# Kernel optimization log

Hardware: AMD Instinct MI355X
Metric: run time of the kernel (lower is better)

## Reference

```python
import jax, jax.numpy as jnp
import numpy as np

N_HEADS = 16
EMBED_DIM = 2048
BATCH, SEQ = 2, 2048


def setup_inputs() -> dict:
    key = jax.random.key(0)
    k1, k2, k3, k4, k5 = jax.random.split(key, 5)
    s_in = 1.0 / np.sqrt(EMBED_DIM)
    return {
        "x": jax.random.normal(k1, (BATCH, SEQ, EMBED_DIM), dtype=jnp.float32),
        "w_in": jax.random.normal(k2, (3 * EMBED_DIM, EMBED_DIM), dtype=jnp.float32) * s_in,
        "b_in": jax.random.normal(k3, (3 * EMBED_DIM,), dtype=jnp.float32) * 0.02,
        "w_out": jax.random.normal(k4, (EMBED_DIM, EMBED_DIM), dtype=jnp.float32) * s_in,
        "b_out": jax.random.normal(k5, (EMBED_DIM,), dtype=jnp.float32) * 0.02,
        "causal_mask": 1,
    }


def reference(x, w_in, b_in, w_out, b_out, causal_mask):
    b, l, e = x.shape
    h, d = N_HEADS, e // N_HEADS
    qkv = x @ w_in.T + b_in                      # [b, l, 3e]
    q, k, v = jnp.split(qkv, 3, axis=-1)
    # b l (h d) -> b h l d
    q = q.reshape(b, l, h, d).transpose(0, 2, 1, 3)
    k = k.reshape(b, l, h, d).transpose(0, 2, 1, 3)
    v = v.reshape(b, l, h, d).transpose(0, 2, 1, 3)
    scores = jnp.einsum("bhqd,bhkd->bhqk", q, k) / jnp.sqrt(jnp.float32(d))
    if causal_mask:
        tri = jnp.triu(jnp.ones((l, l), dtype=bool), k=1)  # True above diagonal
        scores = jnp.where(tri, -jnp.inf, scores)
    attn = jax.nn.softmax(scores, axis=-1)
    out = jnp.einsum("bhqk,bhkd->bhqd", attn, v)  # [b, h, l, d]
    out = out.transpose(0, 2, 1, 3).reshape(b, l, e)
    return out @ w_out.T + b_out
```

## Files before the change

kernel.cpp:

```cpp
#include <hip/hip_runtime.h>
#include <hip/hip_bf16.h>
#include <math.h>

typedef __attribute__((ext_vector_type(4))) float floatx4;
typedef __attribute__((ext_vector_type(16))) float floatx16;
typedef __attribute__((ext_vector_type(8))) __bf16 bf16x8;

__device__ __forceinline__ unsigned short f2bf(float f) {
    union { float f; unsigned int u; } v; v.f = f;
    unsigned int u = v.u;
    u += 0x7FFFu + ((u >> 16) & 1u);
    return (unsigned short)(u >> 16);
}

__device__ __forceinline__ unsigned int pkbf(float a, float b) {
    return (unsigned int)f2bf(a) | ((unsigned int)f2bf(b) << 16);
}

__device__ __forceinline__ void gl_lds16(const void* g, void* l) {
    __builtin_amdgcn_global_load_lds(
        (const __attribute__((address_space(1))) void*)g,
        (__attribute__((address_space(3))) void*)l, 16, 0, 0);
}

__global__ void cast_f32_bf16(const float* __restrict__ in,
                              unsigned short* __restrict__ out, int n) {
    int i = (blockIdx.x * blockDim.x + threadIdx.x) * 4;
    if (i + 4 <= n) {
        float4 f = *(const float4*)(in + i);
        ushort4 o;
        o.x = f2bf(f.x); o.y = f2bf(f.y); o.z = f2bf(f.z); o.w = f2bf(f.w);
        *(ushort4*)(out + i) = o;
    }
}

#define BM 128
#define BN 128
#define BK 32
#define GROUP_M 8

template<int MODE>
__global__ __launch_bounds__(256) void gemm_nt(
    const unsigned short* __restrict__ A,
    const unsigned short* __restrict__ B,
    const float* __restrict__ bias,
    float* __restrict__ Cf,
    unsigned short* __restrict__ q_ws,
    unsigned short* __restrict__ k_ws,
    unsigned short* __restrict__ vT_ws,
    int M, int N, int K)
{
    __shared__ unsigned short Asm[BM][BK];
    __shared__ unsigned short Bsm[BN][BK];

    const int id = blockIdx.x + gridDim.x * blockIdx.y;
    const int perGroup = gridDim.x * GROUP_M;
    const int group = id / perGroup;
    const int rem = id % perGroup;
    const int gh = min(GROUP_M, (int)gridDim.y - group * GROUP_M);
    const int by = group * GROUP_M + rem % gh;
    const int bx = rem / gh;

    const int m0 = by * BM, n0 = bx * BN;
    const int tid = threadIdx.x;
    const int lane = tid & 63, wid = tid >> 6;
    const int quad = lane >> 4, li = lane & 15;
    const int wy = wid >> 1, wx = wid & 1;

    const int lrow = lane >> 2;
    const int lcol = (lane & 3) * 8;

    floatx4 acc[4][4] = {};

    const int kTiles = K / BK;
    for (int kt = 0; kt < kTiles; ++kt) {
        const int k0 = kt * BK;
        #pragma unroll
        for (int c = 0; c < 2; ++c) {
            const int cidx = wid * 2 + c;
            const int row = cidx * 16 + lrow;
            gl_lds16(A + (size_t)(m0 + row) * K + k0 + lcol,
                     &Asm[0][0] + cidx * 512);
            gl_lds16(B + (size_t)(n0 + row) * K + k0 + lcol,
                     &Bsm[0][0] + cidx * 512);
        }
        __syncthreads();

        bf16x8 af[4], bfr[4];
        #pragma unroll
        for (int t = 0; t < 4; ++t) {
            af[t]  = *(const bf16x8*)(&Asm[wy * 64 + t * 16 + li][quad * 8]);
            bfr[t] = *(const bf16x8*)(&Bsm[wx * 64 + t * 16 + li][quad * 8]);
        }
        #pragma unroll
        for (int i = 0; i < 4; ++i)
            #pragma unroll
            for (int j = 0; j < 4; ++j)
                acc[i][j] = __builtin_amdgcn_mfma_f32_16x16x32_bf16(
                    af[i], bfr[j], acc[i][j], 0, 0, 0);
        __syncthreads();
    }

    if (MODE == 0) {
        #pragma unroll
        for (int i = 0; i < 4; ++i)
            #pragma unroll
            for (int j = 0; j < 4; ++j) {
                int col = wx * 64 + j * 16 + li;
                float bv = bias[n0 + col];
                #pragma unroll
                for (int r = 0; r < 4; ++r) {
                    int row = wy * 64 + i * 16 + quad * 4 + r;
                    Cf[(size_t)(m0 + row) * N + n0 + col] = acc[i][j][r] + bv;
                }
            }
    } else {
        const int which = bx >> 4;
        const int h = bx & 15;
        const int b = by >> 4;
        const int lbase = (by & 15) * BM;
        const size_t bh = (size_t)(b * 16 + h);
        #pragma unroll
        for (int i = 0; i < 4; ++i)
            #pragma unroll
            for (int j = 0; j < 4; ++j) {
                int col = wx * 64 + j * 16 + li;
                float bv = bias[n0 + col];
                #pragma unroll
                for (int r = 0; r < 4; ++r) {
                    int row = wy * 64 + i * 16 + quad * 4 + r;
                    int l = lbase + row;
                    unsigned short ob = f2bf(acc[i][j][r] + bv);
                    if (which == 0)      q_ws[(bh * 2048 + l) * 128 + col] = ob;
                    else if (which == 1) k_ws[(bh * 2048 + l) * 128 + col] = ob;
                    else                 vT_ws[(bh * 128 + col) * 2048 + l] = ob;
                }
            }
    }
}

#define AP 8
__global__ __launch_bounds__(256, 2) void attn_kernel(
    const unsigned short* __restrict__ q_ws,
    const unsigned short* __restrict__ k_ws,
    const unsigned short* __restrict__ vT_ws,
    unsigned short* __restrict__ aout,
    const int* __restrict__ causal_ptr)
{
    __shared__ unsigned short Ksm[128][128 + AP];
    __shared__ unsigned short Vsm[128][128 + AP];

    const int ord = blockIdx.x;
    int qt, bhid;
    if (ord < 256) { qt = ord >> 5;              bhid = ord & 31; }
    else           { qt = 15 - ((ord - 256) >> 5); bhid = ord & 31; }
    const int b = bhid >> 4, h = bhid & 15;

    const int tid = threadIdx.x;
    const int lane = tid & 63, w = tid >> 6;
    const int lq = lane & 31;
    const int half = lane >> 5;
    const size_t bh = (size_t)(b * 16 + h);
    const unsigned short* Qp = q_ws + bh * 2048 * 128;
    const unsigned short* Kp = k_ws + bh * 2048 * 128;
    const unsigned short* Vp = vT_ws + bh * 128 * 2048;
    const int causal = causal_ptr[0];
    const float scale = 0.08838834764831845f;

    const int qg = qt * 128 + w * 32 + lq;
    bf16x8 qf[8];
    #pragma unroll
    for (int s = 0; s < 8; ++s)
        qf[s] = *(const bf16x8*)(Qp + (size_t)qg * 128 + s * 16 + half * 8);

    floatx16 O[4] = {};
    float m_i = -INFINITY, l_i = 0.f;

    const int myEnd = causal ? qt : 15;
    for (int kt = 0; kt <= myEnd; ++kt) {
        #pragma unroll
        for (int c = 0; c < 8; ++c) {
            int chunk = c * 256 + tid;
            int row = chunk >> 4;
            int cc  = (chunk & 15) * 8;
            *(uint4*)(&Ksm[row][cc]) =
                *(const uint4*)(Kp + (size_t)(kt * 128 + row) * 128 + cc);
            *(uint4*)(&Vsm[row][cc]) =
                *(const uint4*)(Vp + (size_t)row * 2048 + kt * 128 + cc);
        }
        __syncthreads();

        floatx16 S[4] = {};
        #pragma unroll
        for (int ct = 0; ct < 4; ++ct)
            #pragma unroll
            for (int s = 0; s < 8; ++s) {
                bf16x8 kf = *(const bf16x8*)(&Ksm[ct * 32 + lq][s * 16 + half * 8]);
                S[ct] = __builtin_amdgcn_mfma_f32_32x32x16_bf16(kf, qf[s], S[ct], 0, 0, 0);
            }

        const bool diag = causal && (kt == qt);
        float mx = -INFINITY;
        #pragma unroll
        for (int ct = 0; ct < 4; ++ct)
            #pragma unroll
            for (int r = 0; r < 16; ++r) {
                float sv = S[ct][r] * scale;
                if (diag) {
                    int key = 32 * ct + (r & 3) + 8 * (r >> 2) + 4 * half;
                    if (kt * 128 + key > qg) sv = -INFINITY;
                }
                S[ct][r] = sv;
                mx = fmaxf(mx, sv);
            }
        mx = fmaxf(mx, __shfl_xor(mx, 32, 64));
        float m_new = fmaxf(m_i, mx);
        float m_use = (m_new == -INFINITY) ? 0.f : m_new;
        float alpha = __expf(m_i - m_use);

        float rs = 0.f;
        #pragma unroll
        for (int ct = 0; ct < 4; ++ct)
            #pragma unroll
            for (int r = 0; r < 16; ++r) {
                float p = __expf(S[ct][r] - m_use);
                S[ct][r] = p;
                rs += p;
            }
        rs += __shfl_xor(rs, 32, 64);
        l_i = l_i * alpha + rs;
        m_i = m_new;
        #pragma unroll
        for (int dt = 0; dt < 4; ++dt)
            #pragma unroll
            for (int r = 0; r < 16; ++r)
                O[dt][r] *= alpha;

        bf16x8 pfr[8];
        #pragma unroll
        for (int ct = 0; ct < 4; ++ct)
            #pragma unroll
            for (int h2 = 0; h2 < 2; ++h2) {
                int base = 8 * h2;
                unsigned int pk0 = pkbf(S[ct][base + 0], S[ct][base + 1]);
                unsigned int pk1 = pkbf(S[ct][base + 2], S[ct][base + 3]);
                unsigned int pk2 = pkbf(S[ct][base + 4], S[ct][base + 5]);
                unsigned int pk3 = pkbf(S[ct][base + 6], S[ct][base + 7]);
                unsigned int x0 = __shfl_xor((int)pk0, 32, 64);
                unsigned int x1 = __shfl_xor((int)pk1, 32, 64);
                unsigned int x2 = __shfl_xor((int)pk2, 32, 64);
                unsigned int x3 = __shfl_xor((int)pk3, 32, 64);
                union { unsigned int u[4]; bf16x8 v; } fr;
                fr.u[0] = half ? x2 : pk0;
                fr.u[1] = half ? x3 : pk1;
                fr.u[2] = half ? pk2 : x0;
                fr.u[3] = half ? pk3 : x1;
                pfr[ct * 2 + h2] = fr.v;
            }

        #pragma unroll
        for (int dt = 0; dt < 4; ++dt)
            #pragma unroll
            for (int s = 0; s < 8; ++s) {
                bf16x8 vf = *(const bf16x8*)(&Vsm[dt * 32 + lq][s * 16 + half * 8]);
                O[dt] = __builtin_amdgcn_mfma_f32_32x32x16_bf16(vf, pfr[s], O[dt], 0, 0, 0);
            }
        __syncthreads();
    }

    const float invl = 1.0f / l_i;
    #pragma unroll
    for (int dt = 0; dt < 4; ++dt)
        #pragma unroll
        for (int g = 0; g < 4; ++g) {
            int dbase = dt * 32 + g * 8 + half * 4;
            ushort4 o4;
            o4.x = f2bf(O[dt][g * 4 + 0] * invl);
            o4.y = f2bf(O[dt][g * 4 + 1] * invl);
            o4.z = f2bf(O[dt][g * 4 + 2] * invl);
            o4.w = f2bf(O[dt][g * 4 + 3] * invl);
            *(ushort4*)(&Ksm[w * 32 + lq][dbase]) = o4;
        }
    __syncthreads();
    #pragma unroll
    for (int c = 0; c < 8; ++c) {
        int chunk = c * 256 + tid;
        int row = chunk >> 4;
        int dc = (chunk & 15) * 8;
        uint4 v = *(const uint4*)(&Ksm[row][dc]);
        *(uint4*)(aout + ((size_t)b * 2048 + qt * 128 + row) * 2048 + h * 128 + dc) = v;
    }
}

extern "C" void kernel_launch(void* const* d_in, const int* in_sizes, int n_in,
                              void* d_out, int out_size, void* d_ws, size_t ws_size,
                              hipStream_t stream) {
    const float* x     = (const float*)d_in[0];
    const float* w_in  = (const float*)d_in[1];
    const float* b_in  = (const float*)d_in[2];
    const float* w_out = (const float*)d_in[3];
    const float* b_out = (const float*)d_in[4];
    const int* causal  = (const int*)d_in[5];

    char* ws = (char*)d_ws;
    unsigned short* xb    = (unsigned short*)ws; ws += (size_t)4096 * 2048 * 2;
    unsigned short* wb    = (unsigned short*)ws; ws += (size_t)6144 * 2048 * 2;
    unsigned short* wob   = (unsigned short*)ws; ws += (size_t)2048 * 2048 * 2;
    unsigned short* q_ws  = (unsigned short*)ws; ws += (size_t)32 * 2048 * 128 * 2;
    unsigned short* k_ws  = (unsigned short*)ws; ws += (size_t)32 * 2048 * 128 * 2;
    unsigned short* vT_ws = (unsigned short*)ws; ws += (size_t)32 * 2048 * 128 * 2;
    unsigned short* aout  = (unsigned short*)ws; ws += (size_t)4096 * 2048 * 2;

    cast_f32_bf16<<<8192, 256, 0, stream>>>(x, xb, 4096 * 2048);
    cast_f32_bf16<<<12288, 256, 0, stream>>>(w_in, wb, 6144 * 2048);
    cast_f32_bf16<<<4096, 256, 0, stream>>>(w_out, wob, 2048 * 2048);

    gemm_nt<1><<<dim3(48, 32), 256, 0, stream>>>(
        xb, wb, b_in, nullptr, q_ws, k_ws, vT_ws, 4096, 6144, 2048);

    attn_kernel<<<512, 256, 0, stream>>>(
        q_ws, k_ws, vT_ws, aout, causal);

    gemm_nt<0><<<dim3(16, 32), 256, 0, stream>>>(
        aout, wob, b_out, (float*)d_out, nullptr, nullptr, nullptr,
        4096, 2048, 2048);
}
```

Measured before the change: 437.8 us.

## Split attention key tile into two halves and drop GEMM group swizzle

The attention inner loop now handles each 128-key tile as two 64-key chunks, each with its own online-softmax update, so only two score accumulators are live at a time. This is meant to cut register pressure. The change also relaxes launch bounds to one block per SIMD and guards m_i against staying at -inf. Separately, the GEMM drops its grouped tile swizzle in favour of plain blockIdx mapping, which may hurt L2 reuse, and the extra rescale pass per chunk adds ALU work.

```diff
diff --git a/kernel.cpp b/kernel.cpp
--- a/kernel.cpp
+++ b/kernel.cpp
@@ -37,7 +37,6 @@
 #define BM 128
 #define BN 128
 #define BK 32
-#define GROUP_M 8
 
 template<int MODE>
 __global__ __launch_bounds__(256) void gemm_nt(
@@ -53,14 +52,7 @@
     __shared__ unsigned short Asm[BM][BK];
     __shared__ unsigned short Bsm[BN][BK];
 
-    const int id = blockIdx.x + gridDim.x * blockIdx.y;
-    const int perGroup = gridDim.x * GROUP_M;
-    const int group = id / perGroup;
-    const int rem = id % perGroup;
-    const int gh = min(GROUP_M, (int)gridDim.y - group * GROUP_M);
-    const int by = group * GROUP_M + rem % gh;
-    const int bx = rem / gh;
-
+    const int bx = blockIdx.x, by = blockIdx.y;
     const int m0 = by * BM, n0 = bx * BN;
     const int tid = threadIdx.x;
     const int lane = tid & 63, wid = tid >> 6;
@@ -140,7 +132,7 @@
 }
 
 #define AP 8
-__global__ __launch_bounds__(256, 2) void attn_kernel(
+__global__ __launch_bounds__(256, 1) void attn_kernel(
     const unsigned short* __restrict__ q_ws,
     const unsigned short* __restrict__ k_ws,
     const unsigned short* __restrict__ vT_ws,
@@ -190,81 +182,87 @@
         }
         __syncthreads();
 
-        floatx16 S[4] = {};
-        #pragma unroll
-        for (int ct = 0; ct < 4; ++ct)
-            #pragma unroll
-            for (int s = 0; s < 8; ++s) {
-                bf16x8 kf = *(const bf16x8*)(&Ksm[ct * 32 + lq][s * 16 + half * 8]);
-                S[ct] = __builtin_amdgcn_mfma_f32_32x32x16_bf16(kf, qf[s], S[ct], 0, 0, 0);
+        const bool diag = causal && (kt == qt);
+        #pragma unroll 1
+        for (int ch = 0; ch < 2; ++ch) {
+            floatx16 S[2] = {};
+            #pragma unroll
+            for (int c2 = 0; c2 < 2; ++c2) {
+                const int ct = ch * 2 + c2;
+                #pragma unroll
+                for (int s = 0; s < 8; ++s) {
+                    bf16x8 kf = *(const bf16x8*)(&Ksm[ct * 32 + lq][s * 16 + half * 8]);
+                    S[c2] = __builtin_amdgcn_mfma_f32_32x32x16_bf16(kf, qf[s], S[c2], 0, 0, 0);
+                }
             }
 
-        const bool diag = causal && (kt == qt);
-        float mx = -INFINITY;
-        #pragma unroll
-        for (int ct = 0; ct < 4; ++ct)
-            #pragma unroll
-            for (int r = 0; r < 16; ++r) {
-                float sv = S[ct][r] * scale;
-                if (diag) {
-                    int key = 32 * ct + (r & 3) + 8 * (r >> 2) + 4 * half;
-                    if (kt * 128 + key > qg) sv = -INFINITY;
-                }
-                S[ct][r] = sv;
-                mx = fmaxf(mx, sv);
-            }
-        mx = fmaxf(mx, __shfl_xor(mx, 32, 64));
-        float m_new = fmaxf(m_i, mx);
-        float m_use = (m_new == -INFINITY) ? 0.f : m_new;
-        float alpha = __expf(m_i - m_use);
-
-        float rs = 0.f;
-        #pragma unroll
-        for (int ct = 0; ct < 4; ++ct)
-            #pragma unroll
-            for (int r = 0; r < 16; ++r) {
-                float p = __expf(S[ct][r] - m_use);
-                S[ct][r] = p;
-                rs += p;
-            }
-        rs += __shfl_xor(rs, 32, 64);
-        l_i = l_i * alpha + rs;
-        m_i = m_new;
-        #pragma unroll
-        for (int dt = 0; dt < 4; ++dt)
-            #pragma unroll
-            for (int r = 0; r < 16; ++r)
-                O[dt][r] *= alpha;
-
-        bf16x8 pfr[8];
-        #pragma unroll
-        for (int ct = 0; ct < 4; ++ct)
-            #pragma unroll
-            for (int h2 = 0; h2 < 2; ++h2) {
-                int base = 8 * h2;
-                unsigned int pk0 = pkbf(S[ct][base + 0], S[ct][base + 1]);
-                unsigned int pk1 = pkbf(S[ct][base + 2], S[ct][base + 3]);
-                unsigned int pk2 = pkbf(S[ct][base + 4], S[ct][base + 5]);
-                unsigned int pk3 = pkbf(S[ct][base + 6], S[ct][base + 7]);
-                unsigned int x0 = __shfl_xor((int)pk0, 32, 64);
-                unsigned int x1 = __shfl_xor((int)pk1, 32, 64);
-                unsigned int x2 = __shfl_xor((int)pk2, 32, 64);
-                unsigned int x3 = __shfl_xor((int)pk3, 32, 64);
-                union { unsigned int u[4]; bf16x8 v; } fr;
-                fr.u[0] = half ? x2 : pk0;
-                fr.u[1] = half ? x3 : pk1;
-                fr.u[2] = half ? pk2 : x0;
-                fr.u[3] = half ? pk3 : x1;
-                pfr[ct * 2 + h2] = fr.v;
-            }
-
-        #pragma unroll
-        for (int dt = 0; dt < 4; ++dt)
-            #pragma unroll
-            for (int s = 0; s < 8; ++s) {
-                bf16x8 vf = *(const bf16x8*)(&Vsm[dt * 32 + lq][s * 16 + half * 8]);
-                O[dt] = __builtin_amdgcn_mfma_f32_32x32x16_bf16(vf, pfr[s], O[dt], 0, 0, 0);
-            }
+            float mx = -INFINITY;
+            #pragma unroll
+            for (int c2 = 0; c2 < 2; ++c2)
+                #pragma unroll
+                for (int r = 0; r < 16; ++r) {
+                    float sv = S[c2][r] * scale;
+                    if (diag) {
+                        int key = 32 * (ch * 2 + c2) + (r & 3) + 8 * (r >> 2) + 4 * half;
+                        if (kt * 128 + key > qg) sv = -INFINITY;
+                    }
+                    S[c2][r] = sv;
+                    mx = fmaxf(mx, sv);
+                }
+            mx = fmaxf(mx, __shfl_xor(mx, 32, 64));
+            float m_new = fmaxf(m_i, mx);
+            float m_use = (m_new == -INFINITY) ? 0.f : m_new;
+            float alpha = __expf(m_i - m_use);
+
+            float rs = 0.f;
+            #pragma unroll
+            for (int c2 = 0; c2 < 2; ++c2)
+                #pragma unroll
+                for (int r = 0; r < 16; ++r) {
+                    float p = __expf(S[c2][r] - m_use);
+                    S[c2][r] = p;
+                    rs += p;
+                }
+            rs += __shfl_xor(rs, 32, 64);
+            l_i = l_i * alpha + rs;
+            m_i = (m_new == -INFINITY) ? m_i : m_new;
+            #pragma unroll
+            for (int dt = 0; dt < 4; ++dt)
+                #pragma unroll
+                for (int r = 0; r < 16; ++r)
+                    O[dt][r] *= alpha;
+
+            bf16x8 pfr[4];
+            #pragma unroll
+            for (int c2 = 0; c2 < 2; ++c2)
+                #pragma unroll
+                for (int h2 = 0; h2 < 2; ++h2) {
+                    int base = 8 * h2;
+                    unsigned int pk0 = pkbf(S[c2][base + 0], S[c2][base + 1]);
+                    unsigned int pk1 = pkbf(S[c2][base + 2], S[c2][base + 3]);
+                    unsigned int pk2 = pkbf(S[c2][base + 4], S[c2][base + 5]);
+                    unsigned int pk3 = pkbf(S[c2][base + 6], S[c2][base + 7]);
+                    unsigned int x0 = __shfl_xor((int)pk0, 32, 64);
+                    unsigned int x1 = __shfl_xor((int)pk1, 32, 64);
+                    unsigned int x2 = __shfl_xor((int)pk2, 32, 64);
+                    unsigned int x3 = __shfl_xor((int)pk3, 32, 64);
+                    union { unsigned int u[4]; bf16x8 v; } fr;
+                    fr.u[0] = half ? x2 : pk0;
+                    fr.u[1] = half ? x3 : pk1;
+                    fr.u[2] = half ? pk2 : x0;
+                    fr.u[3] = half ? pk3 : x1;
+                    pfr[c2 * 2 + h2] = fr.v;
+                }
+
+            #pragma unroll
+            for (int dt = 0; dt < 4; ++dt)
+                #pragma unroll
+                for (int p = 0; p < 4; ++p) {
+                    int s = ch * 4 + p;
+                    bf16x8 vf = *(const bf16x8*)(&Vsm[dt * 32 + lq][s * 16 + half * 8]);
+                    O[dt] = __builtin_amdgcn_mfma_f32_32x32x16_bf16(vf, pfr[p], O[dt], 0, 0, 0);
+                }
+        }
         __syncthreads();
     }
 
```

New measurement: 446.2 us. Within noise of the previous version (+1.9%).
